# Kernel optimization log

Measured on AMD Instinct MI355X. Metric: run time of the kernel, lower is better.

The kernel has to match this reference:

```python
import jax, jax.numpy as jnp
import numpy as np

BETA = 0.5
IGNORE_INDEX = -100
TEMPERATURE = 1.0

N, H, V = 2048, 4096, 32000


def setup_inputs() -> dict:
    key = jax.random.key(0)
    k1, k2, k3, k4, k5 = jax.random.split(key, 5)
    scale_s = 1.0 / np.sqrt(H // 2)
    scale_t = 1.0 / np.sqrt(H)
    return {
        "student": jax.random.normal(k1, (N, H // 2), dtype=jnp.float32),
        "W_s": jax.random.normal(k2, (V, H // 2), dtype=jnp.float32) * scale_s,
        "teacher": jax.random.normal(k3, (N, H), dtype=jnp.float32),
        "W_t": jax.random.normal(k4, (V, H), dtype=jnp.float32) * scale_t,
        "target": jax.random.randint(k5, (N,), 0, V, dtype=jnp.int64),
    }


def reference(student, W_s, teacher, W_t, target):
    # Fused linear + JSD: logits are [N, V] (the huge intermediates Liger avoids
    # materializing by chunking over N).
    s_logits = (student @ W_s.T) / TEMPERATURE          # [N, V]  student -> Q
    t_logits = (teacher @ W_t.T) / TEMPERATURE          # [N, V]  teacher -> P
    log_q = jax.nn.log_softmax(s_logits, axis=-1)
    log_p = jax.nn.log_softmax(t_logits, axis=-1)
    p = jnp.exp(log_p)
    q = jnp.exp(log_q)
    # Generalized JSD(beta): beta*KL(P||M) + (1-beta)*KL(Q||M), M = beta*P + (1-beta)*Q
    m = BETA * p + (1.0 - BETA) * q
    log_m = jnp.log(m)
    per_tok = (BETA * jnp.sum(p * (log_p - log_m), axis=-1)
               + (1.0 - BETA) * jnp.sum(q * (log_q - log_m), axis=-1))  # [N]
    mask = target != IGNORE_INDEX
    n_non_ignore = jnp.maximum(jnp.sum(mask), 1)
    loss = jnp.sum(jnp.where(mask, per_tok, 0.0)) / n_non_ignore.astype(per_tok.dtype)
    return loss
```

## Files before the change

### kernel.cpp

```cpp
#include <hip/hip_runtime.h>
#include <hip/hip_bf16.h>
#include <hip/hip_fp8.h>
#include <stdint.h>

#define BETA 0.5f
#define IGNORE_INDEX (-100)
#define WSCALE 64.0f
#define SCALE_ONE  0x7F7F7F7Fu
#define SCALE_D64  0x79797979u

typedef float f32x4 __attribute__((ext_vector_type(4)));
typedef int   i32x4 __attribute__((ext_vector_type(4)));
typedef int   i32x8 __attribute__((ext_vector_type(8)));

__global__ __launch_bounds__(256) void fused_cvt_kernel(
    const float* __restrict__ s0, uint8_t* __restrict__ d0, int e0,
    const float* __restrict__ s1, uint8_t* __restrict__ d1, int e1,
    const float* __restrict__ s2, uint8_t* __restrict__ d2, int e2,
    const float* __restrict__ s3, uint8_t* __restrict__ d3) {
  int b = blockIdx.x;
  const float* src;
  uint8_t* dst;
  float scale;
  if (b < e0)      { src = s0; dst = d0; scale = 1.0f;   }
  else if (b < e1) { src = s1; dst = d1; scale = WSCALE; b -= e0; }
  else if (b < e2) { src = s2; dst = d2; scale = 1.0f;   b -= e1; }
  else             { src = s3; dst = d3; scale = WSCALE; b -= e2; }

  const size_t blk = (size_t)b * 4096;
  const int t4 = threadIdx.x * 4;
  float4 v0 = *reinterpret_cast<const float4*>(src + blk + t4);
  float4 v1 = *reinterpret_cast<const float4*>(src + blk + t4 + 1024);
  float4 v2 = *reinterpret_cast<const float4*>(src + blk + t4 + 2048);
  float4 v3 = *reinterpret_cast<const float4*>(src + blk + t4 + 3072);

  auto pack4 = [&scale](const float4& v) -> uint32_t {
    int r = 0;
    r = __builtin_amdgcn_cvt_pk_fp8_f32(v.x * scale, v.y * scale, r, false);
    r = __builtin_amdgcn_cvt_pk_fp8_f32(v.z * scale, v.w * scale, r, true);
    return (uint32_t)r;
  };
  *reinterpret_cast<uint32_t*>(dst + blk + t4)        = pack4(v0);
  *reinterpret_cast<uint32_t*>(dst + blk + t4 + 1024) = pack4(v1);
  *reinterpret_cast<uint32_t*>(dst + blk + t4 + 2048) = pack4(v2);
  *reinterpret_cast<uint32_t*>(dst + blk + t4 + 3072) = pack4(v3);
}

__global__ __launch_bounds__(512, 2) void gemm_mx3_kernel(
    const uint8_t* __restrict__ At, const uint8_t* __restrict__ Bt,
    uint16_t* __restrict__ Ct, int Kt,
    const uint8_t* __restrict__ As_, const uint8_t* __restrict__ Bs_,
    uint16_t* __restrict__ Cs, int Ks,
    int V, int RT, int CT) {
  __shared__ __align__(16) uint8_t lds[131072];

  const int half = RT * CT;
  const uint8_t *A, *B;
  uint16_t* C;
  int K, bidx = blockIdx.x;
  if (bidx < half) { A = At; B = Bt; C = Ct; K = Kt; }
  else             { A = As_; B = Bs_; C = Cs; K = Ks; bidx -= half; }

  int L = ((half & 7) == 0) ? ((bidx & 7) * (half >> 3) + (bidx >> 3)) : bidx;
  const int rt = L % RT;
  const int ct = L / RT;
  const int row0 = rt * 256;
  const int col0 = ct * 256;

  const int i  = threadIdx.x;
  const int w  = i >> 6;
  const int l  = i & 63;
  const int wl = l & 15;
  const int kg = l >> 4;
  const int wr = w >> 2;
  const int wc = w & 3;

  const int nJ = K >> 7;

  const int rg = i >> 2;
  const int pq = i & 3;
  const int qlog = pq ^ ((rg >> 1) & 3);
  const uint8_t* aSrc = A + (size_t)(row0 + rg) * K + qlog * 16;
  const uint8_t* bSrc = B + (size_t)(col0 + rg) * K + qlog * 16;
  uint8_t* ldsu = lds;

#define GL(srcp, dstp)                                                     \
  __builtin_amdgcn_global_load_lds(                                        \
      (const __attribute__((address_space(1))) void*)(srcp),               \
      (__attribute__((address_space(3))) void*)(dstp), 16, 0, 0)

#define STAGE_A(TT)                                                        \
  do {                                                                     \
    const uint8_t* _s = aSrc + (size_t)(TT) * 64;                          \
    uint8_t* _d = ldsu + (((TT) & 3) * 32768) + i * 16;                    \
    GL(_s, _d); GL(_s + (size_t)128 * K, _d + 8192);                       \
  } while (0)

#define STAGE_B(TT)                                                        \
  do {                                                                     \
    const uint8_t* _s = bSrc + (size_t)(TT) * 64;                          \
    uint8_t* _d = ldsu + (((TT) & 3) * 32768) + 16384 + i * 16;            \
    GL(_s, _d); GL(_s + (size_t)128 * K, _d + 8192);                       \
  } while (0)

  int offA[8], offB[4];
  const int qsw = (kg ^ ((wl >> 1) & 3)) * 16;
#pragma unroll
  for (int m = 0; m < 8; ++m) {
    const int r = wr * 128 + m * 16 + wl;
    offA[m] = r * 64 + qsw;
  }
#pragma unroll
  for (int n = 0; n < 4; ++n) {
    const int r = wc * 64 + n * 16 + wl;
    offB[n] = 16384 + r * 64 + qsw;
  }

  f32x4 acc[8][4] = {};
  i32x8 bF[4];

#define LOADA(dst, mm)                                                     \
  do {                                                                     \
    i32x4 _e = *reinterpret_cast<const i32x4*>(bufE + offA[mm]);           \
    i32x4 _o = *reinterpret_cast<const i32x4*>(bufO + offA[mm]);           \
    dst[0] = _e[0]; dst[1] = _e[1]; dst[2] = _e[2]; dst[3] = _e[3];        \
    dst[4] = _o[0]; dst[5] = _o[1]; dst[6] = _o[2]; dst[7] = _o[3];        \
  } while (0)

  STAGE_A(0); STAGE_B(0); STAGE_A(1); STAGE_B(1);
  if (nJ > 1) {
    STAGE_A(2); STAGE_B(2); STAGE_A(3); STAGE_B(3);
    asm volatile("s_waitcnt vmcnt(8)" ::: "memory");
  } else {
    asm volatile("s_waitcnt vmcnt(0)" ::: "memory");
  }
  __builtin_amdgcn_s_barrier();
  __builtin_amdgcn_sched_barrier(0);

  for (int j = 0; j < nJ; ++j) {
    const uint8_t* bufE = lds + ((2 * j) & 3) * 32768;
    const uint8_t* bufO = lds + ((2 * j + 1) & 3) * 32768;
    const bool stg2 = (j + 2) < nJ;

#pragma unroll
    for (int n = 0; n < 4; ++n) {
      i32x4 be = *reinterpret_cast<const i32x4*>(bufE + offB[n]);
      i32x4 bo = *reinterpret_cast<const i32x4*>(bufO + offB[n]);
      bF[n][0] = be[0]; bF[n][1] = be[1]; bF[n][2] = be[2]; bF[n][3] = be[3];
      bF[n][4] = bo[0]; bF[n][5] = bo[1]; bF[n][6] = bo[2]; bF[n][7] = bo[3];
    }

    if (stg2) {
      STAGE_A(2 * j + 4); STAGE_B(2 * j + 4);
      STAGE_A(2 * j + 5); STAGE_B(2 * j + 5);
    }

    __builtin_amdgcn_s_setprio(1);
    {
      i32x8 aCur, aNxt;
      LOADA(aCur, 0);
#pragma unroll
      for (int m = 0; m < 8; ++m) {
        if (m + 1 < 8) LOADA(aNxt, m + 1);
#pragma unroll
        for (int n = 0; n < 4; ++n)
          acc[m][n] = __builtin_amdgcn_mfma_scale_f32_16x16x128_f8f6f4(
              aCur, bF[n], acc[m][n], 0, 0, 0, SCALE_ONE, 0, SCALE_D64);
        aCur = aNxt;
      }
    }
    __builtin_amdgcn_s_setprio(0);

    if (stg2) {
      asm volatile("s_waitcnt vmcnt(8)" ::: "memory");
    } else {
      asm volatile("s_waitcnt vmcnt(0)" ::: "memory");
    }
    __builtin_amdgcn_s_barrier();
    __builtin_amdgcn_sched_barrier(0);
  }

#pragma unroll
  for (int mg = 0; mg < 8; ++mg)
#pragma unroll
    for (int ng = 0; ng < 4; ++ng)
#pragma unroll
      for (int r = 0; r < 4; ++r) {
        const int row = row0 + wr * 128 + mg * 16 + kg * 4 + r;
        const int col = col0 + wc * 64 + ng * 16 + wl;
        __hip_bfloat16 bv = __float2bfloat16(acc[mg][ng][r]);
        C[(size_t)row * V + col] = *reinterpret_cast<const uint16_t*>(&bv);
      }
#undef LOADA
#undef STAGE_A
#undef STAGE_B
#undef GL
}

__device__ __forceinline__ void unpack8(uint4 v, float* f) {
  uint32_t w[4] = {v.x, v.y, v.z, v.w};
#pragma unroll
  for (int j = 0; j < 4; ++j) {
    union { uint32_t u; float x; } lo, hi;
    lo.u = (w[j] & 0xffffu) << 16;
    hi.u = w[j] & 0xffff0000u;
    f[2 * j] = lo.x;
    f[2 * j + 1] = hi.x;
  }
}

__device__ __forceinline__ float blockReduce(float v, float* sh) {
#pragma unroll
  for (int o = 32; o >= 1; o >>= 1) v += __shfl_xor(v, o, 64);
  const int w = threadIdx.x >> 6;
  __syncthreads();
  if ((threadIdx.x & 63) == 0) sh[w] = v;
  __syncthreads();
  float r = sh[0];
#pragma unroll
  for (int i = 1; i < 4; ++i) r += sh[i];
  return r;
}

__global__ __launch_bounds__(256) void jsd_rows_kernel(
    const uint16_t* __restrict__ SL, const uint16_t* __restrict__ TL,
    float* __restrict__ per_tok, int V) {
  __shared__ __align__(16) uint16_t rowS[32000];
  __shared__ __align__(16) uint16_t rowT[32000];
  __shared__ float redM[2][4], redS[2][4], red[4];

  const int t = threadIdx.x;
  const int row = blockIdx.x;
  const uint4* gS = reinterpret_cast<const uint4*>(SL + (size_t)row * V);
  const uint4* gT = reinterpret_cast<const uint4*>(TL + (size_t)row * V);
  uint4* lS = reinterpret_cast<uint4*>(rowS);
  uint4* lT = reinterpret_cast<uint4*>(rowT);
  const int nvec = V >> 3;

  float mS = -3.0e38f, sS = 0.f, mT = -3.0e38f, sT = 0.f;
  for (int i = t; i < nvec; i += 256) {
    uint4 vs = gS[i], vt = gT[i];
    lS[i] = vs; lT[i] = vt;
    float fs[8], ft[8];
    unpack8(vs, fs);
    unpack8(vt, ft);
    float vmS = fs[0], vmT = ft[0];
#pragma unroll
    for (int j = 1; j < 8; ++j) { vmS = fmaxf(vmS, fs[j]); vmT = fmaxf(vmT, ft[j]); }
    if (vmS > mS) { sS *= __expf(mS - vmS); mS = vmS; }
    if (vmT > mT) { sT *= __expf(mT - vmT); mT = vmT; }
#pragma unroll
    for (int j = 0; j < 8; ++j) { sS += __expf(fs[j] - mS); sT += __expf(ft[j] - mT); }
  }

#pragma unroll
  for (int o = 32; o >= 1; o >>= 1) {
    float mo = __shfl_xor(mS, o, 64), so = __shfl_xor(sS, o, 64);
    float mn = fmaxf(mS, mo);
    sS = sS * __expf(mS - mn) + so * __expf(mo - mn); mS = mn;
    mo = __shfl_xor(mT, o, 64); so = __shfl_xor(sT, o, 64);
    mn = fmaxf(mT, mo);
    sT = sT * __expf(mT - mn) + so * __expf(mo - mn); mT = mn;
  }
  const int wv = t >> 6;
  if ((t & 63) == 0) {
    redM[0][wv] = mS; redS[0][wv] = sS;
    redM[1][wv] = mT; redS[1][wv] = sT;
  }
  __syncthreads();
  float M0 = redM[0][0], S0 = redS[0][0];
  float M1 = redM[1][0], S1 = redS[1][0];
#pragma unroll
  for (int k = 1; k < 4; ++k) {
    float m2 = redM[0][k], s2 = redS[0][k];
    float mn = fmaxf(M0, m2);
    S0 = S0 * __expf(M0 - mn) + s2 * __expf(m2 - mn); M0 = mn;
    m2 = redM[1][k]; s2 = redS[1][k];
    mn = fmaxf(M1, m2);
    S1 = S1 * __expf(M1 - mn) + s2 * __expf(m2 - mn); M1 = mn;
  }
  const float lseS = M0 + __logf(S0);
  const float lseT = M1 + __logf(S1);

  float acc = 0.f;
  for (int i = t; i < nvec; i += 256) {
    float fs[8], ft[8];
    unpack8(lS[i], fs);
    unpack8(lT[i], ft);
#pragma unroll
    for (int j = 0; j < 8; ++j) {
      const float lq = fs[j] - lseS;
      const float lp = ft[j] - lseT;
      const float q = __expf(lq);
      const float p = __expf(lp);
      const float m = BETA * p + (1.f - BETA) * q;
      const float lm = __logf(m);
      acc += BETA * p * (lp - lm) + (1.f - BETA) * q * (lq - lm);
    }
  }
  acc = blockReduce(acc, red);
  if (t == 0) per_tok[row] = acc;
}

__global__ __launch_bounds__(256) void finalize_kernel(
    const float* __restrict__ per_tok, const int* __restrict__ tgt,
    float* __restrict__ out, int N) {
  __shared__ float redf[4];
  __shared__ int redi[4];
  float s = 0.f;
  int c = 0;
  for (int i = threadIdx.x; i < N; i += 256) {
    if (tgt[i] != IGNORE_INDEX) { s += per_tok[i]; c += 1; }
  }
#pragma unroll
  for (int o = 32; o >= 1; o >>= 1) {
    s += __shfl_xor(s, o, 64);
    c += __shfl_xor(c, o, 64);
  }
  const int w = threadIdx.x >> 6;
  if ((threadIdx.x & 63) == 0) { redf[w] = s; redi[w] = c; }
  __syncthreads();
  if (threadIdx.x == 0) {
    float st = 0.f;
    int ct = 0;
#pragma unroll
    for (int i = 0; i < 4; ++i) { st += redf[i]; ct += redi[i]; }
    out[0] = st / (float)(ct > 0 ? ct : 1);
  }
}

extern "C" void kernel_launch(void* const* d_in, const int* in_sizes, int n_in,
                              void* d_out, int out_size, void* d_ws, size_t ws_size,
                              hipStream_t stream) {
  const float* student = (const float*)d_in[0];
  const float* W_s     = (const float*)d_in[1];
  const float* teacher = (const float*)d_in[2];
  const float* W_t     = (const float*)d_in[3];
  const int*   target  = (const int*)d_in[4];

  const int N  = in_sizes[4];
  const int Hs = in_sizes[0] / N;
  const int Ht = in_sizes[2] / N;
  const int V  = in_sizes[1] / Hs;

  char* ws = (char*)d_ws;
  size_t off = 0;
  auto alloc = [&](size_t bytes) -> void* {
    void* p = ws + off;
    off += (bytes + 255) & ~(size_t)255;
    return p;
  };
  uint8_t* Sf8  = (uint8_t*)alloc((size_t)N * Hs);
  uint8_t* Wsf8 = (uint8_t*)alloc((size_t)V * Hs);
  uint8_t* Tf8  = (uint8_t*)alloc((size_t)N * Ht);
  uint8_t* Wtf8 = (uint8_t*)alloc((size_t)V * Ht);
  uint16_t* slog = (uint16_t*)alloc((size_t)N * V * 2);
  uint16_t* tlog = (uint16_t*)alloc((size_t)N * V * 2);
  float* per_tok = (float*)alloc((size_t)N * sizeof(float));
  (void)ws_size;

  const int b0 = (N * Hs) / 4096;
  const int b1 = b0 + (V * Hs) / 4096;
  const int b2 = b1 + (N * Ht) / 4096;
  const int bT = b2 + (V * Ht) / 4096;
  fused_cvt_kernel<<<bT, 256, 0, stream>>>(
      student, Sf8, b0, W_s, Wsf8, b1, teacher, Tf8, b2, W_t, Wtf8);

  const int RT = N / 256;
  const int CT = V / 256;
  gemm_mx3_kernel<<<2 * RT * CT, 512, 0, stream>>>(
      Tf8, Wtf8, tlog, Ht, Sf8, Wsf8, slog, Hs, V, RT, CT);

  jsd_rows_kernel<<<N, 256, 0, stream>>>(slog, tlog, per_tok, V);
  finalize_kernel<<<1, 256, 0, stream>>>(per_tok, target, (float*)d_out, N);
}
```

Before: 729.1 us.

## Use grid-stride nontemporal fp8 conversion and restructure GEMM LDS into double-buffered pairs

The conversion kernel becomes a grid-stride loop over a fixed grid of 4096 blocks. Each thread converts 8 float4 chunks per iteration and reads them with nontemporal loads. The GEMM's LDS staging changes from a 4-slot ring with a prefetch depth of two k-steps to two 64KB halves, each holding one k-pair of A and B. It now waits on vmcnt(0) every iteration. This simplifies addressing and wait counts, but the prefetch distance shrinks, so global-to-LDS latency may be exposed.

```diff
diff --git a/kernel.cpp b/kernel.cpp
--- a/kernel.cpp
+++ b/kernel.cpp
@@ -17,36 +17,35 @@
     const float* __restrict__ s0, uint8_t* __restrict__ d0, int e0,
     const float* __restrict__ s1, uint8_t* __restrict__ d1, int e1,
     const float* __restrict__ s2, uint8_t* __restrict__ d2, int e2,
-    const float* __restrict__ s3, uint8_t* __restrict__ d3) {
-  int b = blockIdx.x;
-  const float* src;
-  uint8_t* dst;
-  float scale;
-  if (b < e0)      { src = s0; dst = d0; scale = 1.0f;   }
-  else if (b < e1) { src = s1; dst = d1; scale = WSCALE; b -= e0; }
-  else if (b < e2) { src = s2; dst = d2; scale = 1.0f;   b -= e1; }
-  else             { src = s3; dst = d3; scale = WSCALE; b -= e2; }
-
-  const size_t blk = (size_t)b * 4096;
-  const int t4 = threadIdx.x * 4;
-  float4 v0 = *reinterpret_cast<const float4*>(src + blk + t4);
-  float4 v1 = *reinterpret_cast<const float4*>(src + blk + t4 + 1024);
-  float4 v2 = *reinterpret_cast<const float4*>(src + blk + t4 + 2048);
-  float4 v3 = *reinterpret_cast<const float4*>(src + blk + t4 + 3072);
-
-  auto pack4 = [&scale](const float4& v) -> uint32_t {
-    int r = 0;
-    r = __builtin_amdgcn_cvt_pk_fp8_f32(v.x * scale, v.y * scale, r, false);
-    r = __builtin_amdgcn_cvt_pk_fp8_f32(v.z * scale, v.w * scale, r, true);
-    return (uint32_t)r;
-  };
-  *reinterpret_cast<uint32_t*>(dst + blk + t4)        = pack4(v0);
-  *reinterpret_cast<uint32_t*>(dst + blk + t4 + 1024) = pack4(v1);
-  *reinterpret_cast<uint32_t*>(dst + blk + t4 + 2048) = pack4(v2);
-  *reinterpret_cast<uint32_t*>(dst + blk + t4 + 3072) = pack4(v3);
-}
-
-__global__ __launch_bounds__(512, 2) void gemm_mx3_kernel(
+    const float* __restrict__ s3, uint8_t* __restrict__ d3, int eT) {
+  for (int c = blockIdx.x; c < eT; c += gridDim.x) {
+    const float* src;
+    uint8_t* dst;
+    float scale;
+    int cb = c;
+    if (c < e0)      { src = s0; dst = d0; scale = 1.0f;   }
+    else if (c < e1) { src = s1; dst = d1; scale = WSCALE; cb -= e0; }
+    else if (c < e2) { src = s2; dst = d2; scale = 1.0f;   cb -= e1; }
+    else             { src = s3; dst = d3; scale = WSCALE; cb -= e2; }
+
+    const size_t base = (size_t)cb * 8192 + threadIdx.x * 4;
+    f32x4 v[8];
+#pragma unroll
+    for (int k = 0; k < 8; ++k)
+      v[k] = __builtin_nontemporal_load(
+          reinterpret_cast<const f32x4*>(src + base + k * 1024));
+#pragma unroll
+    for (int k = 0; k < 8; ++k) {
+      int r = 0;
+      r = __builtin_amdgcn_cvt_pk_fp8_f32(v[k][0] * scale, v[k][1] * scale, r, false);
+      r = __builtin_amdgcn_cvt_pk_fp8_f32(v[k][2] * scale, v[k][3] * scale, r, true);
+      *reinterpret_cast<uint32_t*>(dst + base + k * 1024) = (uint32_t)r;
+    }
+  }
+}
+
+
+__global__ __launch_bounds__(512, 2) void gemm_mx4_kernel(
     const uint8_t* __restrict__ At, const uint8_t* __restrict__ Bt,
     uint16_t* __restrict__ Ct, int Kt,
     const uint8_t* __restrict__ As_, const uint8_t* __restrict__ Bs_,
@@ -89,18 +88,19 @@
       (const __attribute__((address_space(1))) void*)(srcp),               \
       (__attribute__((address_space(3))) void*)(dstp), 16, 0, 0)
 
-#define STAGE_A(TT)                                                        \
+#define STAGE_PAIR(P)                                                      \
   do {                                                                     \
-    const uint8_t* _s = aSrc + (size_t)(TT) * 64;                          \
-    uint8_t* _d = ldsu + (((TT) & 3) * 32768) + i * 16;                    \
-    GL(_s, _d); GL(_s + (size_t)128 * K, _d + 8192);                       \
-  } while (0)
-
-#define STAGE_B(TT)                                                        \
-  do {                                                                     \
-    const uint8_t* _s = bSrc + (size_t)(TT) * 64;                          \
-    uint8_t* _d = ldsu + (((TT) & 3) * 32768) + 16384 + i * 16;            \
-    GL(_s, _d); GL(_s + (size_t)128 * K, _d + 8192);                       \
+    const size_t _kE = (size_t)(2 * (P)) * 64;                             \
+    const size_t _kO = (size_t)(2 * (P) + 1) * 64;                         \
+    uint8_t* _sb = ldsu + (((P) & 1) * 65536);                             \
+    GL(aSrc + _kE, _sb + i * 16);                                          \
+    GL(aSrc + _kE + (size_t)128 * K, _sb + i * 16 + 8192);                 \
+    GL(aSrc + _kO, _sb + 16384 + i * 16);                                  \
+    GL(aSrc + _kO + (size_t)128 * K, _sb + 16384 + i * 16 + 8192);         \
+    GL(bSrc + _kE, _sb + 32768 + i * 16);                                  \
+    GL(bSrc + _kE + (size_t)128 * K, _sb + 32768 + i * 16 + 8192);         \
+    GL(bSrc + _kO, _sb + 49152 + i * 16);                                  \
+    GL(bSrc + _kO + (size_t)128 * K, _sb + 49152 + i * 16 + 8192);         \
   } while (0)
 
   int offA[8], offB[4];
@@ -113,7 +113,7 @@
 #pragma unroll
   for (int n = 0; n < 4; ++n) {
     const int r = wc * 64 + n * 16 + wl;
-    offB[n] = 16384 + r * 64 + qsw;
+    offB[n] = 32768 + r * 64 + qsw;
   }
 
   f32x4 acc[8][4] = {};
@@ -121,39 +121,29 @@
 
 #define LOADA(dst, mm)                                                     \
   do {                                                                     \
-    i32x4 _e = *reinterpret_cast<const i32x4*>(bufE + offA[mm]);           \
-    i32x4 _o = *reinterpret_cast<const i32x4*>(bufO + offA[mm]);           \
+    i32x4 _e = *reinterpret_cast<const i32x4*>(sb + offA[mm]);             \
+    i32x4 _o = *reinterpret_cast<const i32x4*>(sb + offA[mm] + 16384);     \
     dst[0] = _e[0]; dst[1] = _e[1]; dst[2] = _e[2]; dst[3] = _e[3];        \
     dst[4] = _o[0]; dst[5] = _o[1]; dst[6] = _o[2]; dst[7] = _o[3];        \
   } while (0)
 
-  STAGE_A(0); STAGE_B(0); STAGE_A(1); STAGE_B(1);
-  if (nJ > 1) {
-    STAGE_A(2); STAGE_B(2); STAGE_A(3); STAGE_B(3);
-    asm volatile("s_waitcnt vmcnt(8)" ::: "memory");
-  } else {
-    asm volatile("s_waitcnt vmcnt(0)" ::: "memory");
-  }
+  STAGE_PAIR(0);
+  asm volatile("s_waitcnt vmcnt(0)" ::: "memory");
   __builtin_amdgcn_s_barrier();
   __builtin_amdgcn_sched_barrier(0);
 
   for (int j = 0; j < nJ; ++j) {
-    const uint8_t* bufE = lds + ((2 * j) & 3) * 32768;
-    const uint8_t* bufO = lds + ((2 * j + 1) & 3) * 32768;
-    const bool stg2 = (j + 2) < nJ;
+    const uint8_t* sb = lds + (j & 1) * 65536;
 
 #pragma unroll
     for (int n = 0; n < 4; ++n) {
-      i32x4 be = *reinterpret_cast<const i32x4*>(bufE + offB[n]);
-      i32x4 bo = *reinterpret_cast<const i32x4*>(bufO + offB[n]);
+      i32x4 be = *reinterpret_cast<const i32x4*>(sb + offB[n]);
+      i32x4 bo = *reinterpret_cast<const i32x4*>(sb + offB[n] + 16384);
       bF[n][0] = be[0]; bF[n][1] = be[1]; bF[n][2] = be[2]; bF[n][3] = be[3];
       bF[n][4] = bo[0]; bF[n][5] = bo[1]; bF[n][6] = bo[2]; bF[n][7] = bo[3];
     }
 
-    if (stg2) {
-      STAGE_A(2 * j + 4); STAGE_B(2 * j + 4);
-      STAGE_A(2 * j + 5); STAGE_B(2 * j + 5);
-    }
+    if (j + 1 < nJ) STAGE_PAIR(j + 1);
 
     __builtin_amdgcn_s_setprio(1);
     {
@@ -171,11 +161,7 @@
     }
     __builtin_amdgcn_s_setprio(0);
 
-    if (stg2) {
-      asm volatile("s_waitcnt vmcnt(8)" ::: "memory");
-    } else {
-      asm volatile("s_waitcnt vmcnt(0)" ::: "memory");
-    }
+    asm volatile("s_waitcnt vmcnt(0)" ::: "memory");
     __builtin_amdgcn_s_barrier();
     __builtin_amdgcn_sched_barrier(0);
   }
@@ -192,8 +178,7 @@
         C[(size_t)row * V + col] = *reinterpret_cast<const uint16_t*>(&bv);
       }
 #undef LOADA
-#undef STAGE_A
-#undef STAGE_B
+#undef STAGE_PAIR
 #undef GL
 }
 
@@ -359,16 +344,16 @@
   float* per_tok = (float*)alloc((size_t)N * sizeof(float));
   (void)ws_size;
 
-  const int b0 = (N * Hs) / 4096;
-  const int b1 = b0 + (V * Hs) / 4096;
-  const int b2 = b1 + (N * Ht) / 4096;
-  const int bT = b2 + (V * Ht) / 4096;
-  fused_cvt_kernel<<<bT, 256, 0, stream>>>(
-      student, Sf8, b0, W_s, Wsf8, b1, teacher, Tf8, b2, W_t, Wtf8);
+  const int c0 = (N * Hs) / 8192;
+  const int c1 = c0 + (V * Hs) / 8192;
+  const int c2 = c1 + (N * Ht) / 8192;
+  const int cT = c2 + (V * Ht) / 8192;
+  fused_cvt_kernel<<<4096, 256, 0, stream>>>(
+      student, Sf8, c0, W_s, Wsf8, c1, teacher, Tf8, c2, W_t, Wtf8, cT);
 
   const int RT = N / 256;
   const int CT = V / 256;
-  gemm_mx3_kernel<<<2 * RT * CT, 512, 0, stream>>>(
+  gemm_mx4_kernel<<<2 * RT * CT, 512, 0, stream>>>(
       Tf8, Wtf8, tlog, Ht, Sf8, Wsf8, slog, Hs, V, RT, CT);
 
   jsd_rows_kernel<<<N, 256, 0, stream>>>(slog, tlog, per_tok, V);
```

New measurement: 725.7 us, median of 2. Within noise of the previous version (-0.5%).
